# Optimization experiments

Measured on AMD Instinct MI355X. Metric: run time of the kernel, lower is better.

The kernel has to match this reference:

```python
import jax, jax.numpy as jnp
import numpy as np

D_MODEL = 1024
N_HEADS = 16
D_K = D_MODEL // N_HEADS  # 64
ROPE_BASE = 10000.0
MASK_FILL = -1e9


def _rope_cos_sin(seq_len, d_k, dtype):
    # inv_freq over even dims, freqs = outer(t, inv_freq): [S, d_k//2]
    inv_freq = 1.0 / (ROPE_BASE ** (jnp.arange(0, d_k, 2, dtype=jnp.float32) / d_k))
    freqs = jnp.arange(seq_len, dtype=jnp.float32)[:, None] * inv_freq[None, :]
    # broadcast to full d_k (rotate_half convention: same freq for x1 and x2 halves)
    cos = jnp.concatenate([jnp.cos(freqs), jnp.cos(freqs)], axis=-1).astype(dtype)
    sin = jnp.concatenate([jnp.sin(freqs), jnp.sin(freqs)], axis=-1).astype(dtype)
    return cos, sin  # each [S, d_k]


def _apply_rope(x, cos, sin):
    # x: [B, H, S, d_k]; rotate_half: (x1, x2) -> (-x2, x1)
    x1, x2 = jnp.split(x, 2, axis=-1)
    rot = jnp.concatenate([-x2, x1], axis=-1)
    return x * cos[None, None] + rot * sin[None, None]


def setup_inputs() -> dict:
    key = jax.random.key(0)
    kx, kqkv, ko = jax.random.split(key, 3)
    x = jax.random.normal(kx, (1, 4096, D_MODEL), dtype=jnp.float32)
    # nn.Linear weight shape [out, in]; y = x @ W.T
    s = 1.0 / np.sqrt(D_MODEL)
    W_qkv = jax.random.uniform(kqkv, (3 * D_MODEL, D_MODEL), jnp.float32, -s, s)
    W_o = jax.random.uniform(ko, (D_MODEL, D_MODEL), jnp.float32, -s, s)
    return {"x": x, "W_qkv": W_qkv, "W_o": W_o}


def reference(x, W_qkv, W_o):
    B, S, _ = x.shape
    qkv = jnp.einsum("bsd,ed->bse", x, W_qkv)  # [B, S, 3*d_model]
    Q, K, V = jnp.split(qkv, 3, axis=-1)
    # [B, S, H, d_k] -> [B, H, S, d_k]
    reshape = lambda t: t.reshape(B, S, N_HEADS, D_K).transpose(0, 2, 1, 3)
    Q, K, V = reshape(Q), reshape(K), reshape(V)
    cos, sin = _rope_cos_sin(S, D_K, x.dtype)
    Q = _apply_rope(Q, cos, sin)
    K = _apply_rope(K, cos, sin)
    scores = jnp.einsum("bhqd,bhkd->bhqk", Q, K) / jnp.sqrt(jnp.asarray(D_K, x.dtype))
    causal = jnp.tril(jnp.ones((S, S), dtype=bool))
    scores = jnp.where(causal[None, None], scores, jnp.asarray(MASK_FILL, x.dtype))
    attn = jax.nn.softmax(scores, axis=-1)  # dropout inactive at inference
    out = jnp.einsum("bhqk,bhkd->bhqd", attn, V)
    out = out.transpose(0, 2, 1, 3).reshape(B, S, D_MODEL)
    return jnp.einsum("bsd,ed->bse", out, W_o)
```

## Files before the change

### kernel.cpp

```cpp
#include <hip/hip_runtime.h>


typedef __attribute__((ext_vector_type(8)))  short  short8;
typedef __attribute__((ext_vector_type(4)))  float  f32x4;
typedef __attribute__((ext_vector_type(16))) float  f32x16;
typedef __attribute__((ext_vector_type(4)))  float  float4v;
typedef __attribute__((ext_vector_type(4)))  unsigned short ushort4v;
typedef __attribute__((ext_vector_type(4)))  unsigned int   uint4v;

#define S_LEN 4096
#define DMODEL 1024
#define NHEADS 16
#define DKH 64

#define QSCALE 0.18033688011112042f

__device__ __forceinline__ unsigned short f2bf(float f) {
  unsigned u = __builtin_bit_cast(unsigned, f);
  u += 0x7FFFu + ((u >> 16) & 1u);
  return (unsigned short)(u >> 16);
}
__device__ __forceinline__ float bf2f(unsigned short h) {
  return __builtin_bit_cast(float, ((unsigned)h) << 16);
}

#define GLDS16(gsrc, ldst)                                                   \
  __builtin_amdgcn_global_load_lds(                                          \
      (const __attribute__((address_space(1))) void*)(gsrc),                 \
      (__attribute__((address_space(3))) void*)(ldst), 16, 0, 0)

__global__ void cvt_bf16_all(const float* __restrict__ x,    unsigned short* __restrict__ xb,
                             const float* __restrict__ wq,   unsigned short* __restrict__ wqb,
                             const float* __restrict__ wo,   unsigned short* __restrict__ wob) {
  int i = blockIdx.x * blockDim.x + threadIdx.x;
  const float* src; unsigned short* dst; int off;
  if (i < 1048576)               { src = x;  dst = xb;  off = i; }
  else if (i < 1048576 + 786432) { src = wq; dst = wqb; off = i - 1048576; }
  else                           { src = wo; dst = wob; off = i - 1048576 - 786432; }
  float4v v = reinterpret_cast<const float4v*>(src)[off];
  ushort4v o;
  o[0] = f2bf(v[0]); o[1] = f2bf(v[1]); o[2] = f2bf(v[2]); o[3] = f2bf(v[3]);
  reinterpret_cast<ushort4v*>(dst)[off] = o;
}

template<bool OUT_BF16>
__global__ __launch_bounds__(256) void gemm_lds(const unsigned short* __restrict__ A,
                                                const unsigned short* __restrict__ B,
                                                void* __restrict__ Cp,
                                                int M, int N, int K) {
  __shared__ __align__(16) unsigned short As[128 * 32];
  __shared__ __align__(16) unsigned short Bs[128 * 32];

  const int tid = threadIdx.x;
  const int l = tid & 63, w = tid >> 6;
  const int wr = w >> 1, wc = w & 1;
  const int bm = blockIdx.y * 128, bn = blockIdx.x * 128;
  const int lr = l & 15, lk = (l >> 4) * 8;

  f32x4 acc[4][4] = {};

  const unsigned short* Ag0 = A + (size_t)(bm + (tid >> 2)) * K + (tid & 3) * 8;
  const unsigned short* Ag1 = A + (size_t)(bm + 64 + (tid >> 2)) * K + (tid & 3) * 8;
  const unsigned short* Bg0 = B + (size_t)(bn + (tid >> 2)) * K + (tid & 3) * 8;
  const unsigned short* Bg1 = B + (size_t)(bn + 64 + (tid >> 2)) * K + (tid & 3) * 8;
  unsigned short* Ad0 = As + tid * 8;
  unsigned short* Ad1 = As + (tid + 256) * 8;
  unsigned short* Bd0 = Bs + tid * 8;
  unsigned short* Bd1 = Bs + (tid + 256) * 8;

  const unsigned short* Afr = As + (wr * 64 + lr) * 32 + lk;
  const unsigned short* Bfr = Bs + (wc * 64 + lr) * 32 + lk;

  for (int k0 = 0; k0 < K; k0 += 32) {
    GLDS16(Ag0 + k0, Ad0);
    GLDS16(Ag1 + k0, Ad1);
    GLDS16(Bg0 + k0, Bd0);
    GLDS16(Bg1 + k0, Bd1);
    __syncthreads();

    short8 af[4], bfr[4];
#pragma unroll
    for (int mi = 0; mi < 4; mi++) af[mi]  = *(const short8*)(Afr + mi * 16 * 32);
#pragma unroll
    for (int ni = 0; ni < 4; ni++) bfr[ni] = *(const short8*)(Bfr + ni * 16 * 32);

#pragma unroll
    for (int mi = 0; mi < 4; mi++)
#pragma unroll
      for (int ni = 0; ni < 4; ni++)
        acc[mi][ni] = __builtin_amdgcn_mfma_f32_16x16x32_bf16(af[mi], bfr[ni],
                                                              acc[mi][ni], 0, 0, 0);
    __syncthreads();
  }

  const int row0 = bm + wr * 64 + (l >> 4) * 4;
  const int col0 = bn + wc * 64 + lr;
#pragma unroll
  for (int mi = 0; mi < 4; mi++)
#pragma unroll
    for (int ni = 0; ni < 4; ni++)
#pragma unroll
      for (int j = 0; j < 4; j++) {
        size_t idx = (size_t)(row0 + mi * 16 + j) * N + (col0 + ni * 16);
        if (OUT_BF16) ((unsigned short*)Cp)[idx] = f2bf(acc[mi][ni][j]);
        else          ((float*)Cp)[idx]          = acc[mi][ni][j];
      }
}

__global__ void rope_split_kernel(const unsigned short* __restrict__ qkv,
                                  unsigned short* __restrict__ Qr,
                                  unsigned short* __restrict__ Kr,
                                  unsigned short* __restrict__ Vt) {
  int gid = blockIdx.x * blockDim.x + threadIdx.x;
  int s = gid >> 9;
  int t = gid & 511;
  int h = t >> 5, d = t & 31;
  int e = h * 64 + d;
  size_t base = (size_t)s * 3072;

  float q1 = bf2f(qkv[base + e]);
  float q2 = bf2f(qkv[base + e + 32]);
  float k1 = bf2f(qkv[base + 1024 + e]);
  float k2 = bf2f(qkv[base + 1024 + e + 32]);

  float inv = expf(-(float)(2 * d) * (9.2103403719761836f / 64.0f));
  float ang = (float)s * inv;
  float sn, cs;
  sincosf(ang, &sn, &cs);

  float qo1 = q1 * cs - q2 * sn, qo2 = q2 * cs + q1 * sn;
  float ko1 = k1 * cs - k2 * sn, ko2 = k2 * cs + k1 * sn;

  size_t o1 = ((size_t)h * S_LEN + s) * DKH + d;
  Qr[o1]      = f2bf(qo1 * QSCALE);
  Qr[o1 + 32] = f2bf(qo2 * QSCALE);
  Kr[o1]      = f2bf(ko1);
  Kr[o1 + 32] = f2bf(ko2);
  Vt[((size_t)h * DKH + d) * S_LEN + s]        = qkv[base + 2048 + e];
  Vt[((size_t)h * DKH + d + 32) * S_LEN + s]   = qkv[base + 2048 + e + 32];
}

__global__ __launch_bounds__(256) void flash_attn_kernel(const unsigned short* __restrict__ Qr,
                                                         const unsigned short* __restrict__ Kr,
                                                         const unsigned short* __restrict__ Vt,
                                                         unsigned short* __restrict__ O) {
  __shared__ __align__(16) char smem[32768];

  const int tid = threadIdx.x;
  const int l  = tid & 63;
  const int w  = tid >> 6;
  const int r  = l & 31;
  const int hi = l >> 5;

  const int bx    = blockIdx.x;
  const int xcd   = bx & 7;
  const int j     = bx >> 3;
  const int h     = xcd * 2 + (j & 1);
  const int qtile = 127 - (j >> 1);
  const int q0    = qtile * 32;

  const unsigned short* Qh = Qr + (size_t)h * S_LEN * DKH;
  const unsigned short* Kh = Kr + (size_t)h * S_LEN * DKH;
  const unsigned short* Vh = Vt + (size_t)h * DKH * S_LEN;

  const int krow  = tid >> 3;
  const int kcE   = (((tid & 7) * 16) ^ ((krow & 7) << 4)) >> 1;
  const size_t kbase = (size_t)krow * DKH + kcE;
  const int vrow  = tid >> 4;
  const int vcE   = (((tid & 15) * 16) ^ ((vrow & 7) << 4)) >> 1;
  const size_t vbase = (size_t)vrow * S_LEN + vcE;

  const int sw      = (r & 7) << 4;
  const int kfbyte  = (w * 32 + r) * 128;
  const int vfbyte0 = r * 256;
  const int vfbyte1 = (r + 32) * 256;
  const int vcol    = w * 64 + hi * 16;

  short8 qf[4];
  {
    const unsigned short* qb = Qh + (size_t)(q0 + r) * 64 + hi * 8;
#pragma unroll
    for (int dc = 0; dc < 4; dc++) qf[dc] = *(const short8*)(qb + dc * 16);
  }

  f32x16 acc0 = {}, acc1 = {};
  float m = -1e30f, lsum = 0.0f;

  const int nwin = (qtile >> 2) + 1;
  for (int it = 0; it < nwin; it++) {
    {
      const unsigned short* Kg = Kh + (size_t)it * 128 * DKH;
      const unsigned short* Vg = Vh + it * 128;
#pragma unroll
      for (int i = 0; i < 4; i++) {
        GLDS16(Kg + kbase + (size_t)i * 32 * DKH, smem + i * 4096 + tid * 16);
        GLDS16(Vg + vbase + (size_t)i * 16 * S_LEN,
               smem + 16384 + i * 4096 + tid * 16);
      }
    }
    __syncthreads();

    const int c = 4 * it + w;
    if (c <= qtile) {
      short8 kf[4], vf[4];
#pragma unroll
      for (int dc = 0; dc < 4; dc++)
        kf[dc] = *(const short8*)(smem + kfbyte + ((dc * 32 + hi * 16) ^ sw));
#pragma unroll
      for (int kc = 0; kc < 2; kc++) {
        vf[kc]     = *(const short8*)(smem + 16384 + vfbyte0 + ((vcol + kc * 32) ^ sw));
        vf[2 + kc] = *(const short8*)(smem + 16384 + vfbyte1 + ((vcol + kc * 32) ^ sw));
      }

      f32x16 st = {};
      __builtin_amdgcn_s_setprio(1);
      st = __builtin_amdgcn_mfma_f32_32x32x16_bf16(kf[0], qf[0], st, 0, 0, 0);
      st = __builtin_amdgcn_mfma_f32_32x32x16_bf16(kf[1], qf[1], st, 0, 0, 0);
      st = __builtin_amdgcn_mfma_f32_32x32x16_bf16(kf[2], qf[2], st, 0, 0, 0);
      st = __builtin_amdgcn_mfma_f32_32x32x16_bf16(kf[3], qf[3], st, 0, 0, 0);
      __builtin_amdgcn_s_setprio(0);

      if (c == qtile) {
#pragma unroll
        for (int reg = 0; reg < 16; reg++) {
          const int koff = (reg & 3) + 8 * (reg >> 2) + 4 * hi;
          if (koff > r) st[reg] = -1e30f;
        }
      }

      float t0 = fmaxf(fmaxf(st[0],  st[1]),  st[2]);
      float t1 = fmaxf(fmaxf(st[3],  st[4]),  st[5]);
      float t2 = fmaxf(fmaxf(st[6],  st[7]),  st[8]);
      float t3 = fmaxf(fmaxf(st[9],  st[10]), st[11]);
      float t4 = fmaxf(fmaxf(st[12], st[13]), st[14]);
      float pm = fmaxf(fmaxf(fmaxf(t0, t1), fmaxf(t2, t3)), fmaxf(t4, st[15]));
      pm = fmaxf(pm, __shfl_xor(pm, 32));

      if (!__all(pm <= m + 8.0f)) {
        float mn  = fmaxf(m, pm);
        float scl = exp2f(m - mn);
        m = mn;
        lsum *= scl;
#pragma unroll
        for (int reg = 0; reg < 16; reg++) { acc0[reg] *= scl; acc1[reg] *= scl; }
      }

      float p[16];
#pragma unroll
      for (int reg = 0; reg < 16; reg++) p[reg] = exp2f(st[reg] - m);

      float s2[8];
#pragma unroll
      for (int i = 0; i < 8; i++) s2[i] = p[2 * i] + p[2 * i + 1];
#pragma unroll
      for (int i = 0; i < 4; i++) s2[i] = s2[i] + s2[i + 4];
      float rs = (s2[0] + s2[2]) + (s2[1] + s2[3]);
      rs += __shfl_xor(rs, 32);
      lsum += rs;

      unsigned wd[8];
#pragma unroll
      for (int i = 0; i < 8; i++) {
        asm("v_cvt_pk_bf16_f32 %0, %1, %2" : "=v"(wd[i]) : "v"(p[2 * i]), "v"(p[2 * i + 1]));
      }
      unsigned pw[8];
#pragma unroll
      for (int i = 0; i < 8; i++) pw[i] = __shfl_xor(wd[i], 32);

      uint4v u0, u1;
      u0[0] = hi ? pw[2] : wd[0];
      u0[1] = hi ? pw[3] : wd[1];
      u0[2] = hi ? wd[2] : pw[0];
      u0[3] = hi ? wd[3] : pw[1];
      u1[0] = hi ? pw[6] : wd[4];
      u1[1] = hi ? pw[7] : wd[5];
      u1[2] = hi ? wd[6] : pw[4];
      u1[3] = hi ? wd[7] : pw[5];
      short8 pa0 = __builtin_bit_cast(short8, u0);
      short8 pa1 = __builtin_bit_cast(short8, u1);

      __builtin_amdgcn_s_setprio(1);
      acc0 = __builtin_amdgcn_mfma_f32_32x32x16_bf16(vf[0], pa0, acc0, 0, 0, 0);
      acc0 = __builtin_amdgcn_mfma_f32_32x32x16_bf16(vf[1], pa1, acc0, 0, 0, 0);
      acc1 = __builtin_amdgcn_mfma_f32_32x32x16_bf16(vf[2], pa0, acc1, 0, 0, 0);
      acc1 = __builtin_amdgcn_mfma_f32_32x32x16_bf16(vf[3], pa1, acc1, 0, 0, 0);
      __builtin_amdgcn_s_setprio(0);
    }
    __syncthreads();
  }

  unsigned (*oaccp)[32][33] = (unsigned (*)[32][33])smem;
  float* mlm = (float*)(smem + 16896);
  float* mll = (float*)(smem + 17408);

  if (hi == 0) { mlm[w * 32 + r] = m; mll[w * 32 + r] = lsum; }
#pragma unroll
  for (int i = 0; i < 8; i++) {
    const int widx = 4 * (i >> 1) + 2 * hi + (i & 1);
    unsigned ua, ub;
    asm("v_cvt_pk_bf16_f32 %0, %1, %2" : "=v"(ua) : "v"(acc0[2 * i]), "v"(acc0[2 * i + 1]));
    asm("v_cvt_pk_bf16_f32 %0, %1, %2" : "=v"(ub) : "v"(acc1[2 * i]), "v"(acc1[2 * i + 1]));
    oaccp[w][r][widx]      = ua;
    oaccp[w][r][16 + widx] = ub;
  }
  __syncthreads();

  const int q  = tid >> 3;
  const int c0 = (tid & 7) * 4;
  const float m0 = mlm[q], m1 = mlm[32 + q], m2 = mlm[64 + q], m3 = mlm[96 + q];
  const float mmax = fmaxf(fmaxf(m0, m1), fmaxf(m2, m3));
  const float sc[4] = {exp2f(m0 - mmax), exp2f(m1 - mmax),
                       exp2f(m2 - mmax), exp2f(m3 - mmax)};
  const float ltot = sc[0] * mll[q] + sc[1] * mll[32 + q] +
                     sc[2] * mll[64 + q] + sc[3] * mll[96 + q];
  const float rinv = 1.0f / ltot;

  float vs[8] = {};
#pragma unroll
  for (int wv = 0; wv < 4; wv++) {
#pragma unroll
    for (int i = 0; i < 4; i++) {
      unsigned u = oaccp[wv][q][c0 + i];
      vs[2 * i]     += sc[wv] * __builtin_bit_cast(float, u << 16);
      vs[2 * i + 1] += sc[wv] * __builtin_bit_cast(float, u & 0xFFFF0000u);
    }
  }
  short8 ov;
#pragma unroll
  for (int i = 0; i < 8; i++) ov[i] = (short)f2bf(vs[i] * rinv);
  *(short8*)(O + (size_t)(q0 + q) * DMODEL + h * 64 + c0 * 2) = ov;
}

extern "C" void kernel_launch(void* const* d_in, const int* in_sizes, int n_in,
                              void* d_out, int out_size, void* d_ws, size_t ws_size,
                              hipStream_t stream) {
  (void)in_sizes; (void)n_in; (void)out_size; (void)ws_size;
  const float* x    = (const float*)d_in[0];
  const float* Wqkv = (const float*)d_in[1];
  const float* Wo   = (const float*)d_in[2];
  float* out = (float*)d_out;

  char* ws = (char*)d_ws;
  const size_t MB = 1u << 20;
  unsigned short* x_bf    = (unsigned short*)(ws + 0 * MB);
  unsigned short* wqkv_bf = (unsigned short*)(ws + 8 * MB);
  unsigned short* wo_bf   = (unsigned short*)(ws + 14 * MB);
  unsigned short* qkv_bf  = (unsigned short*)(ws + 16 * MB);
  unsigned short* Qr      = (unsigned short*)(ws + 40 * MB);
  unsigned short* Kr      = (unsigned short*)(ws + 48 * MB);
  unsigned short* Vt      = (unsigned short*)(ws + 56 * MB);
  unsigned short* Obf     = (unsigned short*)(ws + 64 * MB);

  cvt_bf16_all<<<8192, 256, 0, stream>>>(x, x_bf, Wqkv, wqkv_bf, Wo, wo_bf);

  gemm_lds<true><<<dim3(3072 / 128, 4096 / 128), 256, 0, stream>>>(x_bf, wqkv_bf, qkv_bf,
                                                                   4096, 3072, 1024);
  rope_split_kernel<<<8192, 256, 0, stream>>>(qkv_bf, Qr, Kr, Vt);

  flash_attn_kernel<<<2048, 256, 0, stream>>>(Qr, Kr, Vt, Obf);

  gemm_lds<false><<<dim3(1024 / 128, 4096 / 128), 256, 0, stream>>>(Obf, wo_bf, out,
                                                                    4096, 1024, 1024);
}
```

Baseline: 191.7 us.

## Fuse RoPE and Q/K head split into QKV GEMM epilogue, tiled V transpose

The QKV GEMM epilogue now applies RoPE from a precomputed cos/sin table and writes Q (scaled) and K directly in head-major layout. V goes to a temporary buffer and is then transposed by a separate LDS-tiled kernel. This removes the full qkv round trip and the standalone rope kernel with its strided, uncoalesced V stores. The cost is scattered 2-byte epilogue stores, table reads, and two extra small launches.

```diff
diff --git a/kernel.cpp b/kernel.cpp
--- a/kernel.cpp
+++ b/kernel.cpp
@@ -43,11 +43,23 @@
   reinterpret_cast<ushort4v*>(dst)[off] = o;
 }
 
-template<bool OUT_BF16>
-__global__ __launch_bounds__(256) void gemm_lds(const unsigned short* __restrict__ A,
+__global__ void rope_table(float2* __restrict__ tab) {
+  int id = blockIdx.x * blockDim.x + threadIdx.x;
+  int s = id >> 5, i = id & 31;
+  float inv = expf(-(float)(2 * i) * (9.2103403719761836f / 64.0f));
+  float ang = (float)s * inv;
+  float sn, cs;
+  sincosf(ang, &sn, &cs);
+  tab[id] = make_float2(cs, sn);
+}
+
+__global__ __launch_bounds__(256) void gemm_qkv(const unsigned short* __restrict__ A,
                                                 const unsigned short* __restrict__ B,
-                                                void* __restrict__ Cp,
-                                                int M, int N, int K) {
+                                                const float2* __restrict__ tab,
+                                                unsigned short* __restrict__ Qr,
+                                                unsigned short* __restrict__ Kr,
+                                                unsigned short* __restrict__ vtmp) {
+  const int K = 1024;
   __shared__ __align__(16) unsigned short As[128 * 32];
   __shared__ __align__(16) unsigned short Bs[128 * 32];
 
@@ -94,50 +106,138 @@
   }
 
   const int row0 = bm + wr * 64 + (l >> 4) * 4;
+  const int region = bn >> 10;
+  if (region < 2) {
+    const int base64 = (bn & 1023) + wc * 64;
+    const int h = base64 >> 6;
+    unsigned short* dst = region ? Kr : Qr;
+    const float scale = region ? 1.0f : QSCALE;
+    const size_t hb = (size_t)h * S_LEN * DKH;
+#pragma unroll
+    for (int mi = 0; mi < 4; mi++)
+#pragma unroll
+      for (int jj = 0; jj < 4; jj++) {
+        const int s = row0 + mi * 16 + jj;
+        const float2 cs0 = tab[s * 32 + lr];
+        const float2 cs1 = tab[s * 32 + lr + 16];
+        const float x1 = acc[mi][0][jj], x2 = acc[mi][2][jj];
+        const float y1 = acc[mi][1][jj], y2 = acc[mi][3][jj];
+        const float o0 = (x1 * cs0.x - x2 * cs0.y) * scale;
+        const float o2 = (x2 * cs0.x + x1 * cs0.y) * scale;
+        const float o1 = (y1 * cs1.x - y2 * cs1.y) * scale;
+        const float o3 = (y2 * cs1.x + y1 * cs1.y) * scale;
+        const size_t a = hb + (size_t)s * DKH + lr;
+        dst[a]      = f2bf(o0);
+        dst[a + 16] = f2bf(o1);
+        dst[a + 32] = f2bf(o2);
+        dst[a + 48] = f2bf(o3);
+      }
+  } else {
+    const int col0 = (bn - 2048) + wc * 64 + lr;
+#pragma unroll
+    for (int mi = 0; mi < 4; mi++)
+#pragma unroll
+      for (int ni = 0; ni < 4; ni++)
+#pragma unroll
+        for (int jj = 0; jj < 4; jj++)
+          vtmp[(size_t)(row0 + mi * 16 + jj) * 1024 + col0 + ni * 16] =
+              f2bf(acc[mi][ni][jj]);
+  }
+}
+
+__global__ __launch_bounds__(256) void gemm_lds_f32(const unsigned short* __restrict__ A,
+                                                    const unsigned short* __restrict__ B,
+                                                    float* __restrict__ Cp,
+                                                    int M, int N, int K) {
+  __shared__ __align__(16) unsigned short As[128 * 32];
+  __shared__ __align__(16) unsigned short Bs[128 * 32];
+
+  const int tid = threadIdx.x;
+  const int l = tid & 63, w = tid >> 6;
+  const int wr = w >> 1, wc = w & 1;
+  const int bm = blockIdx.y * 128, bn = blockIdx.x * 128;
+  const int lr = l & 15, lk = (l >> 4) * 8;
+
+  f32x4 acc[4][4] = {};
+
+  const unsigned short* Ag0 = A + (size_t)(bm + (tid >> 2)) * K + (tid & 3) * 8;
+  const unsigned short* Ag1 = A + (size_t)(bm + 64 + (tid >> 2)) * K + (tid & 3) * 8;
+  const unsigned short* Bg0 = B + (size_t)(bn + (tid >> 2)) * K + (tid & 3) * 8;
+  const unsigned short* Bg1 = B + (size_t)(bn + 64 + (tid >> 2)) * K + (tid & 3) * 8;
+  unsigned short* Ad0 = As + tid * 8;
+  unsigned short* Ad1 = As + (tid + 256) * 8;
+  unsigned short* Bd0 = Bs + tid * 8;
+  unsigned short* Bd1 = Bs + (tid + 256) * 8;
+
+  const unsigned short* Afr = As + (wr * 64 + lr) * 32 + lk;
+  const unsigned short* Bfr = Bs + (wc * 64 + lr) * 32 + lk;
+
+  for (int k0 = 0; k0 < K; k0 += 32) {
+    GLDS16(Ag0 + k0, Ad0);
+    GLDS16(Ag1 + k0, Ad1);
+    GLDS16(Bg0 + k0, Bd0);
+    GLDS16(Bg1 + k0, Bd1);
+    __syncthreads();
+
+    short8 af[4], bfr[4];
+#pragma unroll
+    for (int mi = 0; mi < 4; mi++) af[mi]  = *(const short8*)(Afr + mi * 16 * 32);
+#pragma unroll
+    for (int ni = 0; ni < 4; ni++) bfr[ni] = *(const short8*)(Bfr + ni * 16 * 32);
+
+#pragma unroll
+    for (int mi = 0; mi < 4; mi++)
+#pragma unroll
+      for (int ni = 0; ni < 4; ni++)
+        acc[mi][ni] = __builtin_amdgcn_mfma_f32_16x16x32_bf16(af[mi], bfr[ni],
+                                                              acc[mi][ni], 0, 0, 0);
+    __syncthreads();
+  }
+
+  const int row0 = bm + wr * 64 + (l >> 4) * 4;
   const int col0 = bn + wc * 64 + lr;
 #pragma unroll
   for (int mi = 0; mi < 4; mi++)
 #pragma unroll
     for (int ni = 0; ni < 4; ni++)
 #pragma unroll
-      for (int j = 0; j < 4; j++) {
-        size_t idx = (size_t)(row0 + mi * 16 + j) * N + (col0 + ni * 16);
-        if (OUT_BF16) ((unsigned short*)Cp)[idx] = f2bf(acc[mi][ni][j]);
-        else          ((float*)Cp)[idx]          = acc[mi][ni][j];
-      }
-}
-
-__global__ void rope_split_kernel(const unsigned short* __restrict__ qkv,
-                                  unsigned short* __restrict__ Qr,
-                                  unsigned short* __restrict__ Kr,
-                                  unsigned short* __restrict__ Vt) {
-  int gid = blockIdx.x * blockDim.x + threadIdx.x;
-  int s = gid >> 9;
-  int t = gid & 511;
-  int h = t >> 5, d = t & 31;
-  int e = h * 64 + d;
-  size_t base = (size_t)s * 3072;
-
-  float q1 = bf2f(qkv[base + e]);
-  float q2 = bf2f(qkv[base + e + 32]);
-  float k1 = bf2f(qkv[base + 1024 + e]);
-  float k2 = bf2f(qkv[base + 1024 + e + 32]);
-
-  float inv = expf(-(float)(2 * d) * (9.2103403719761836f / 64.0f));
-  float ang = (float)s * inv;
-  float sn, cs;
-  sincosf(ang, &sn, &cs);
-
-  float qo1 = q1 * cs - q2 * sn, qo2 = q2 * cs + q1 * sn;
-  float ko1 = k1 * cs - k2 * sn, ko2 = k2 * cs + k1 * sn;
-
-  size_t o1 = ((size_t)h * S_LEN + s) * DKH + d;
-  Qr[o1]      = f2bf(qo1 * QSCALE);
-  Qr[o1 + 32] = f2bf(qo2 * QSCALE);
-  Kr[o1]      = f2bf(ko1);
-  Kr[o1 + 32] = f2bf(ko2);
-  Vt[((size_t)h * DKH + d) * S_LEN + s]        = qkv[base + 2048 + e];
-  Vt[((size_t)h * DKH + d + 32) * S_LEN + s]   = qkv[base + 2048 + e + 32];
+      for (int j = 0; j < 4; j++)
+        Cp[(size_t)(row0 + mi * 16 + j) * N + (col0 + ni * 16)] = acc[mi][ni][j];
+}
+
+__global__ __launch_bounds__(256) void v_transpose(const unsigned short* __restrict__ vtmp,
+                                                   unsigned short* __restrict__ Vt) {
+  __shared__ unsigned lds[64 * 65];
+  const int t  = threadIdx.x;
+  const int b  = blockIdx.x;
+  const int h  = b >> 6;
+  const int s0 = (b & 63) * 64;
+
+  const int sl = t >> 2;
+  const int cq = (t & 3) * 16;
+  {
+    const unsigned short* src = vtmp + (size_t)(s0 + sl) * 1024 + h * 64 + cq;
+    short8 v0 = *(const short8*)(src);
+    short8 v1 = *(const short8*)(src + 8);
+#pragma unroll
+    for (int jj = 0; jj < 8; jj++) {
+      lds[sl * 65 + cq + jj]     = (unsigned short)v0[jj];
+      lds[sl * 65 + cq + 8 + jj] = (unsigned short)v1[jj];
+    }
+  }
+  __syncthreads();
+
+  const int dl = t >> 2;
+  const int sq = (t & 3) * 16;
+  short8 o0, o1;
+#pragma unroll
+  for (int k = 0; k < 8; k++) {
+    o0[k] = (short)(unsigned short)lds[(sq + k) * 65 + dl];
+    o1[k] = (short)(unsigned short)lds[(sq + 8 + k) * 65 + dl];
+  }
+  unsigned short* dst = Vt + (size_t)(h * 64 + dl) * S_LEN + s0 + sq;
+  *(short8*)(dst)     = o0;
+  *(short8*)(dst + 8) = o1;
 }
 
 __global__ __launch_bounds__(256) void flash_attn_kernel(const unsigned short* __restrict__ Qr,
@@ -345,20 +445,22 @@
   unsigned short* x_bf    = (unsigned short*)(ws + 0 * MB);
   unsigned short* wqkv_bf = (unsigned short*)(ws + 8 * MB);
   unsigned short* wo_bf   = (unsigned short*)(ws + 14 * MB);
-  unsigned short* qkv_bf  = (unsigned short*)(ws + 16 * MB);
+  unsigned short* vtmp    = (unsigned short*)(ws + 16 * MB);
+  float2*         tab     = (float2*)(ws + 24 * MB);
   unsigned short* Qr      = (unsigned short*)(ws + 40 * MB);
   unsigned short* Kr      = (unsigned short*)(ws + 48 * MB);
   unsigned short* Vt      = (unsigned short*)(ws + 56 * MB);
   unsigned short* Obf     = (unsigned short*)(ws + 64 * MB);
 
   cvt_bf16_all<<<8192, 256, 0, stream>>>(x, x_bf, Wqkv, wqkv_bf, Wo, wo_bf);
-
-  gemm_lds<true><<<dim3(3072 / 128, 4096 / 128), 256, 0, stream>>>(x_bf, wqkv_bf, qkv_bf,
-                                                                   4096, 3072, 1024);
-  rope_split_kernel<<<8192, 256, 0, stream>>>(qkv_bf, Qr, Kr, Vt);
+  rope_table<<<512, 256, 0, stream>>>(tab);
+
+  gemm_qkv<<<dim3(3072 / 128, 4096 / 128), 256, 0, stream>>>(x_bf, wqkv_bf, tab,
+                                                             Qr, Kr, vtmp);
+  v_transpose<<<1024, 256, 0, stream>>>(vtmp, Vt);
 
   flash_attn_kernel<<<2048, 256, 0, stream>>>(Qr, Kr, Vt, Obf);
 
-  gemm_lds<false><<<dim3(1024 / 128, 4096 / 128), 256, 0, stream>>>(Obf, wo_bf, out,
-                                                                    4096, 1024, 1024);
-}
+  gemm_lds_f32<<<dim3(1024 / 128, 4096 / 128), 256, 0, stream>>>(Obf, wo_bf, out,
+                                                                 4096, 1024, 1024);
+}
```

New measurement: 185.4 us. 3.3% less time.
